# Optimization experiments

Measured on AMD Instinct MI355X. Metric: run time of the kernel, lower is better.

The kernel has to match this reference:

```python
import jax, jax.numpy as jnp
import numpy as np

N_NODES = 50000
N_EDGES = 800000
IN_CH, HID_CH, OUT_CH, HEADS = 64, 32, 64, 8
NEG_SLOPE = 0.2


def setup_inputs() -> dict:
    key = jax.random.key(0)
    ks = jax.random.split(key, 12)
    x = jax.random.normal(ks[0], (N_NODES, IN_CH), dtype=jnp.float32)
    src = jax.random.randint(ks[1], (N_EDGES,), 0, N_NODES)
    dst = jax.random.randint(ks[2], (N_EDGES,), 0, N_NODES)
    edge_index = jnp.stack([src, dst]).astype(jnp.int64)
    g1 = 1.0 / np.sqrt(IN_CH)
    g2 = 1.0 / np.sqrt(HID_CH * HEADS)
    W1 = jax.random.normal(ks[3], (IN_CH, HEADS * HID_CH), dtype=jnp.float32) * g1
    a1_src = jax.random.normal(ks[4], (HEADS, HID_CH), dtype=jnp.float32) * g1
    a1_dst = jax.random.normal(ks[5], (HEADS, HID_CH), dtype=jnp.float32) * g1
    b1 = jnp.zeros((HEADS * HID_CH,), dtype=jnp.float32)
    W2 = jax.random.normal(ks[6], (HEADS * HID_CH, OUT_CH), dtype=jnp.float32) * g2
    a2_src = jax.random.normal(ks[7], (1, OUT_CH), dtype=jnp.float32) * g2
    a2_dst = jax.random.normal(ks[8], (1, OUT_CH), dtype=jnp.float32) * g2
    b2 = jnp.zeros((OUT_CH,), dtype=jnp.float32)
    return {"x": x, "edge_index": edge_index, "W1": W1, "a1_src": a1_src,
            "a1_dst": a1_dst, "b1": b1, "W2": W2, "a2_src": a2_src,
            "a2_dst": a2_dst, "b2": b2}


def _gat_conv(x, src, dst, W, a_s, a_d, b, heads, out_ch, concat):
    """PyG GATConv: per-head linear, edge attention, segment softmax, scatter-add."""
    n = x.shape[0]
    h = (x @ W).reshape(n, heads, out_ch)                    # [N,H,C]
    al_s = jnp.einsum('nhc,hc->nh', h, a_s)                  # [N,H]
    al_d = jnp.einsum('nhc,hc->nh', h, a_d)
    e = jax.nn.leaky_relu(al_s[src] + al_d[dst], NEG_SLOPE)  # [E,H]
    m = jax.ops.segment_max(e, dst, num_segments=n)          # [N,H]
    m = jnp.where(jnp.isfinite(m), m, 0.0)
    ex = jnp.exp(e - m[dst])
    denom = jax.ops.segment_sum(ex, dst, num_segments=n)
    alpha = ex / (denom[dst] + 1e-16)                        # [E,H]
    msg = h[src] * alpha[:, :, None]                         # [E,H,C]
    out = jax.ops.segment_sum(msg, dst, num_segments=n)      # [N,H,C]
    out = out.reshape(n, heads * out_ch) if concat else out.mean(axis=1)
    return out + b


def reference(x, edge_index, W1, a1_src, a1_dst, b1, W2, a2_src, a2_dst, b2):
    n = x.shape[0]
    loops = jnp.arange(n, dtype=edge_index.dtype)
    src = jnp.concatenate([edge_index[0], loops])  # self-loops (PyG default)
    dst = jnp.concatenate([edge_index[1], loops])
    h = _gat_conv(x, src, dst, W1, a1_src, a1_dst, b1, HEADS, HID_CH, True)
    h = jax.nn.elu(h)
    return _gat_conv(h, src, dst, W2, a2_src, a2_dst, b2, 1, OUT_CH, False)
```

## Files before the change

kernel.cpp:

```cpp
#include <hip/hip_runtime.h>
#include <hip/hip_fp16.h>

#define NEG_SLOPE 0.2f
#define CAP 64
#define EPB 4096
#define CAP_B 2560

__global__ __launch_bounds__(256, 4) void k_phase1(
    const int* __restrict__ ei, int E,
    const float* __restrict__ x, const float* __restrict__ W1,
    const float* __restrict__ a1s, const float* __restrict__ a1d,
    __half* __restrict__ h1h, float* __restrict__ al1s, float* __restrict__ al1d,
    int* __restrict__ cursor, unsigned* __restrict__ pairs,
    int n, int nbuck, int nP1B)
{
  __shared__ int sh[2048];
  int t = threadIdx.x;
  if (blockIdx.x < nP1B) {
    int* hist = sh;
    int* hbase = sh + 512;
    for (int i = t; i < nbuck; i += 256) hist[i] = 0;
    __syncthreads();
    int ebase = blockIdx.x * EPB;
    int pk[16], bk[16], rk[16];
#pragma unroll
    for (int k = 0; k < 16; k++) {
      int eid = ebase + k * 256 + t;
      bk[k] = -1; pk[k] = 0; rk[k] = 0;
      if (eid < E) {
        int s = ei[eid], d = ei[E + eid];
        s = (s < 0) ? 0 : (s >= n ? n - 1 : s);
        d = (d < 0) ? 0 : (d >= n ? n - 1 : d);
        bk[k] = d >> 7;
        pk[k] = ((d & 127) << 17) | s;
        rk[k] = atomicAdd(&hist[d >> 7], 1);
      }
    }
    __syncthreads();
    for (int b = t; b < nbuck; b += 256) {
      int c = hist[b];
      hbase[b] = c ? atomicAdd(&cursor[b], c) : 0;
    }
    __syncthreads();
#pragma unroll
    for (int k = 0; k < 16; k++) {
      if (bk[k] >= 0) {
        int idx = hbase[bk[k]] + rk[k];
        if (idx < CAP_B)
          pairs[(size_t)bk[k] * CAP_B + idx] = (unsigned)pk[k];
      }
    }
    return;
  }
  float (*xs)[64] = reinterpret_cast<float(*)[64]>(sh);
  int cg = t & 63;
  int mg = t >> 6;
  int base = (blockIdx.x - nP1B) * 32;
  for (int i = t; i < 32 * 16; i += 256) {
    int m = i >> 4, k4 = i & 15;
    int node = base + m;
    float4 v = make_float4(0.f, 0.f, 0.f, 0.f);
    if (node < n) v = reinterpret_cast<const float4*>(x + (size_t)node * 64)[k4];
    reinterpret_cast<float4*>(&xs[m][0])[k4] = v;
  }
  float4 as4 = reinterpret_cast<const float4*>(a1s)[cg];
  float4 ad4 = reinterpret_cast<const float4*>(a1d)[cg];
  __syncthreads();
  float4 acc[8];
#pragma unroll
  for (int m = 0; m < 8; m++) acc[m] = make_float4(0.f, 0.f, 0.f, 0.f);
#pragma unroll 1
  for (int k4 = 0; k4 < 16; k4++) {
    float4 w0 = reinterpret_cast<const float4*>(W1 + (size_t)(4 * k4 + 0) * 256)[cg];
    float4 w1 = reinterpret_cast<const float4*>(W1 + (size_t)(4 * k4 + 1) * 256)[cg];
    float4 w2 = reinterpret_cast<const float4*>(W1 + (size_t)(4 * k4 + 2) * 256)[cg];
    float4 w3 = reinterpret_cast<const float4*>(W1 + (size_t)(4 * k4 + 3) * 256)[cg];
#pragma unroll
    for (int m = 0; m < 8; m++) {
      float4 xv = reinterpret_cast<float4*>(&xs[mg * 8 + m][0])[k4];
      acc[m].x = fmaf(xv.x, w0.x, acc[m].x); acc[m].y = fmaf(xv.x, w0.y, acc[m].y);
      acc[m].z = fmaf(xv.x, w0.z, acc[m].z); acc[m].w = fmaf(xv.x, w0.w, acc[m].w);
      acc[m].x = fmaf(xv.y, w1.x, acc[m].x); acc[m].y = fmaf(xv.y, w1.y, acc[m].y);
      acc[m].z = fmaf(xv.y, w1.z, acc[m].z); acc[m].w = fmaf(xv.y, w1.w, acc[m].w);
      acc[m].x = fmaf(xv.z, w2.x, acc[m].x); acc[m].y = fmaf(xv.z, w2.y, acc[m].y);
      acc[m].z = fmaf(xv.z, w2.z, acc[m].z); acc[m].w = fmaf(xv.z, w2.w, acc[m].w);
      acc[m].x = fmaf(xv.w, w3.x, acc[m].x); acc[m].y = fmaf(xv.w, w3.y, acc[m].y);
      acc[m].z = fmaf(xv.w, w3.z, acc[m].z); acc[m].w = fmaf(xv.w, w3.w, acc[m].w);
    }
  }
#pragma unroll
  for (int m = 0; m < 8; m++) {
    int node = base + mg * 8 + m;
    if (node < n) {
      __half2 p01 = __floats2half2_rn(acc[m].x, acc[m].y);
      __half2 p23 = __floats2half2_rn(acc[m].z, acc[m].w);
      uint2 pko;
      pko.x = *reinterpret_cast<unsigned int*>(&p01);
      pko.y = *reinterpret_cast<unsigned int*>(&p23);
      reinterpret_cast<uint2*>(h1h + (size_t)node * 256)[cg] = pko;
      float s_ = acc[m].x * as4.x + acc[m].y * as4.y + acc[m].z * as4.z + acc[m].w * as4.w;
      float d_ = acc[m].x * ad4.x + acc[m].y * ad4.y + acc[m].z * ad4.z + acc[m].w * ad4.w;
      s_ += __shfl_xor(s_, 1); d_ += __shfl_xor(d_, 1);
      s_ += __shfl_xor(s_, 2); d_ += __shfl_xor(d_, 2);
      s_ += __shfl_xor(s_, 4); d_ += __shfl_xor(d_, 4);
      if ((cg & 7) == 0) {
        al1s[node * 8 + (cg >> 3)] = s_;
        al1d[node * 8 + (cg >> 3)] = d_;
      }
    }
  }
}

__global__ __launch_bounds__(256) void k_pass2(
    const unsigned* __restrict__ pairs, const int* __restrict__ cursor,
    int* __restrict__ deg, int* __restrict__ esrc, int n)
{
  __shared__ int cnt[128];
  int b = blockIdx.x, t = threadIdx.x;
  if (t < 128) cnt[t] = 0;
  __syncthreads();
  int total = min(cursor[b], CAP_B);
  size_t base = (size_t)b * CAP_B;
  for (int i = t; i < total; i += 256) {
    unsigned p = pairs[base + i];
    int s = p & 0x1FFFF;
    int local = p >> 17;
    int slot = atomicAdd(&cnt[local], 1);
    if (slot < CAP) esrc[((b << 7) + local) * CAP + slot] = s;
  }
  __syncthreads();
  if (t < 128) {
    int node = (b << 7) + t;
    if (node < n) deg[node] = min(cnt[t], CAP);
  }
}

__global__ __launch_bounds__(256, 4) void k_linear2(
    const __half* __restrict__ hacth, const float* __restrict__ W2,
    const float* __restrict__ a2s, const float* __restrict__ a2d,
    __half* __restrict__ h2h, float* __restrict__ al2s, float* __restrict__ al2d,
    int n)
{
  __shared__ float xs[32][260];
  int t = threadIdx.x;
  int cg = t & 15;
  int mg = t >> 4;
  int base = blockIdx.x * 32;
  for (int i = t; i < 32 * 32; i += 256) {
    int m = i >> 5, c8 = i & 31;
    int node = base + m;
    uint4 pk = make_uint4(0, 0, 0, 0);
    if (node < n) pk = reinterpret_cast<const uint4*>(hacth + (size_t)node * 256)[c8];
    __half2* hp = reinterpret_cast<__half2*>(&pk);
    float2 f0 = __half22float2(hp[0]);
    float2 f1 = __half22float2(hp[1]);
    float2 f2 = __half22float2(hp[2]);
    float2 f3 = __half22float2(hp[3]);
    float4* dst = reinterpret_cast<float4*>(&xs[m][c8 * 8]);
    dst[0] = make_float4(f0.x, f0.y, f1.x, f1.y);
    dst[1] = make_float4(f2.x, f2.y, f3.x, f3.y);
  }
  float4 as4 = reinterpret_cast<const float4*>(a2s)[cg];
  float4 ad4 = reinterpret_cast<const float4*>(a2d)[cg];
  __syncthreads();
  float4 a0 = make_float4(0.f, 0.f, 0.f, 0.f);
  float4 a1 = make_float4(0.f, 0.f, 0.f, 0.f);
#pragma unroll 2
  for (int k4 = 0; k4 < 64; k4++) {
    float4 w0 = reinterpret_cast<const float4*>(W2 + (size_t)(4 * k4 + 0) * 64)[cg];
    float4 w1 = reinterpret_cast<const float4*>(W2 + (size_t)(4 * k4 + 1) * 64)[cg];
    float4 w2 = reinterpret_cast<const float4*>(W2 + (size_t)(4 * k4 + 2) * 64)[cg];
    float4 w3 = reinterpret_cast<const float4*>(W2 + (size_t)(4 * k4 + 3) * 64)[cg];
    float4 x0 = *reinterpret_cast<float4*>(&xs[2 * mg + 0][k4 * 4]);
    float4 x1 = *reinterpret_cast<float4*>(&xs[2 * mg + 1][k4 * 4]);
    a0.x = fmaf(x0.x, w0.x, a0.x); a0.y = fmaf(x0.x, w0.y, a0.y);
    a0.z = fmaf(x0.x, w0.z, a0.z); a0.w = fmaf(x0.x, w0.w, a0.w);
    a0.x = fmaf(x0.y, w1.x, a0.x); a0.y = fmaf(x0.y, w1.y, a0.y);
    a0.z = fmaf(x0.y, w1.z, a0.z); a0.w = fmaf(x0.y, w1.w, a0.w);
    a0.x = fmaf(x0.z, w2.x, a0.x); a0.y = fmaf(x0.z, w2.y, a0.y);
    a0.z = fmaf(x0.z, w2.z, a0.z); a0.w = fmaf(x0.z, w2.w, a0.w);
    a0.x = fmaf(x0.w, w3.x, a0.x); a0.y = fmaf(x0.w, w3.y, a0.y);
    a0.z = fmaf(x0.w, w3.z, a0.z); a0.w = fmaf(x0.w, w3.w, a0.w);
    a1.x = fmaf(x1.x, w0.x, a1.x); a1.y = fmaf(x1.x, w0.y, a1.y);
    a1.z = fmaf(x1.x, w0.z, a1.z); a1.w = fmaf(x1.x, w0.w, a1.w);
    a1.x = fmaf(x1.y, w1.x, a1.x); a1.y = fmaf(x1.y, w1.y, a1.y);
    a1.z = fmaf(x1.y, w1.z, a1.z); a1.w = fmaf(x1.y, w1.w, a1.w);
    a1.x = fmaf(x1.z, w2.x, a1.x); a1.y = fmaf(x1.z, w2.y, a1.y);
    a1.z = fmaf(x1.z, w2.z, a1.z); a1.w = fmaf(x1.z, w2.w, a1.w);
    a1.x = fmaf(x1.w, w3.x, a1.x); a1.y = fmaf(x1.w, w3.y, a1.y);
    a1.z = fmaf(x1.w, w3.z, a1.z); a1.w = fmaf(x1.w, w3.w, a1.w);
  }
#pragma unroll
  for (int nd = 0; nd < 2; nd++) {
    float4 a = nd ? a1 : a0;
    int node = base + 2 * mg + nd;
    if (node < n) {
      __half2 q0 = __floats2half2_rn(a.x, a.y);
      __half2 q1 = __floats2half2_rn(a.z, a.w);
      uint2 pk;
      pk.x = *reinterpret_cast<unsigned int*>(&q0);
      pk.y = *reinterpret_cast<unsigned int*>(&q1);
      reinterpret_cast<uint2*>(h2h + (size_t)node * 64)[cg] = pk;
      float s_ = a.x * as4.x + a.y * as4.y + a.z * as4.z + a.w * as4.w;
      float d_ = a.x * ad4.x + a.y * ad4.y + a.z * ad4.z + a.w * ad4.w;
      s_ += __shfl_xor(s_, 1); d_ += __shfl_xor(d_, 1);
      s_ += __shfl_xor(s_, 2); d_ += __shfl_xor(d_, 2);
      s_ += __shfl_xor(s_, 4); d_ += __shfl_xor(d_, 4);
      s_ += __shfl_xor(s_, 8); d_ += __shfl_xor(d_, 8);
      if (cg == 0) { al2s[node] = s_; al2d[node] = d_; }
    }
  }
}

__global__ __launch_bounds__(256) void k_gather1(
    const __half* __restrict__ h1h, const float* __restrict__ al1s, const float* __restrict__ al1d,
    const int* __restrict__ degv, const int* __restrict__ esrc,
    const float* __restrict__ b1, __half* __restrict__ hacth, int n)
{
  int node = blockIdx.x * 16 + (threadIdx.x >> 4);
  if (node >= n) return;
  int q = threadIdx.x & 15;
  int head = q >> 1;
  int beg = node * CAP;
  int deg = min(degv[node], CAP);
  float ald = al1d[node * 8 + head];
  const uint4* rowN = reinterpret_cast<const uint4*>(h1h + (size_t)node * 256);
  uint4 n0 = rowN[2 * q], n1 = rowN[2 * q + 1];
  float eS = al1s[node * 8 + head] + ald;
  eS = eS > 0.f ? eS : NEG_SLOPE * eS;
  float exS = __expf(eS);
  float acc[16];
#pragma unroll
  for (int k = 0; k < 16; k++) acc[k] = 0.f;
  float den = 0.f;
  if (deg > 0) {
    int sA = esrc[beg];
    float alA = al1s[sA * 8 + head];
    const uint4* rowA = reinterpret_cast<const uint4*>(h1h + (size_t)sA * 256);
    uint4 pa0 = rowA[2 * q], pa1 = rowA[2 * q + 1];
    for (int i = 0; i < deg; i++) {
      float alB = 0.f;
      uint4 pb0 = make_uint4(0, 0, 0, 0), pb1 = make_uint4(0, 0, 0, 0);
      if (i + 1 < deg) {
        int sB = esrc[beg + i + 1];
        alB = al1s[sB * 8 + head];
        const uint4* rowB = reinterpret_cast<const uint4*>(h1h + (size_t)sB * 256);
        pb0 = rowB[2 * q]; pb1 = rowB[2 * q + 1];
      }
      float e = alA + ald;
      e = e > 0.f ? e : NEG_SLOPE * e;
      float ex = __expf(e);
      den += ex;
      __half2* hp0 = reinterpret_cast<__half2*>(&pa0);
      __half2* hp1 = reinterpret_cast<__half2*>(&pa1);
#pragma unroll
      for (int j = 0; j < 4; j++) {
        float2 f0 = __half22float2(hp0[j]);
        float2 f1 = __half22float2(hp1[j]);
        acc[2 * j + 0] = fmaf(ex, f0.x, acc[2 * j + 0]);
        acc[2 * j + 1] = fmaf(ex, f0.y, acc[2 * j + 1]);
        acc[8 + 2 * j + 0] = fmaf(ex, f1.x, acc[8 + 2 * j + 0]);
        acc[8 + 2 * j + 1] = fmaf(ex, f1.y, acc[8 + 2 * j + 1]);
      }
      alA = alB; pa0 = pb0; pa1 = pb1;
    }
  }
  den += exS;
  {
    __half2* hp0 = reinterpret_cast<__half2*>(&n0);
    __half2* hp1 = reinterpret_cast<__half2*>(&n1);
#pragma unroll
    for (int j = 0; j < 4; j++) {
      float2 f0 = __half22float2(hp0[j]);
      float2 f1 = __half22float2(hp1[j]);
      acc[2 * j + 0] = fmaf(exS, f0.x, acc[2 * j + 0]);
      acc[2 * j + 1] = fmaf(exS, f0.y, acc[2 * j + 1]);
      acc[8 + 2 * j + 0] = fmaf(exS, f1.x, acc[8 + 2 * j + 0]);
      acc[8 + 2 * j + 1] = fmaf(exS, f1.y, acc[8 + 2 * j + 1]);
    }
  }
  float inv = 1.f / (den + 1e-16f);
  float o[16];
#pragma unroll
  for (int j = 0; j < 4; j++) {
    float4 b4 = reinterpret_cast<const float4*>(b1)[4 * q + j];
    o[4 * j + 0] = acc[4 * j + 0] * inv + b4.x;
    o[4 * j + 1] = acc[4 * j + 1] * inv + b4.y;
    o[4 * j + 2] = acc[4 * j + 2] * inv + b4.z;
    o[4 * j + 3] = acc[4 * j + 3] * inv + b4.w;
  }
#pragma unroll
  for (int k = 0; k < 16; k++) o[k] = o[k] > 0.f ? o[k] : (__expf(o[k]) - 1.f);
  uint4 w0, w1;
  __half2 t0, t1;
  t0 = __floats2half2_rn(o[0], o[1]);  w0.x = *reinterpret_cast<unsigned int*>(&t0);
  t1 = __floats2half2_rn(o[2], o[3]);  w0.y = *reinterpret_cast<unsigned int*>(&t1);
  t0 = __floats2half2_rn(o[4], o[5]);  w0.z = *reinterpret_cast<unsigned int*>(&t0);
  t1 = __floats2half2_rn(o[6], o[7]);  w0.w = *reinterpret_cast<unsigned int*>(&t1);
  t0 = __floats2half2_rn(o[8], o[9]);  w1.x = *reinterpret_cast<unsigned int*>(&t0);
  t1 = __floats2half2_rn(o[10], o[11]); w1.y = *reinterpret_cast<unsigned int*>(&t1);
  t0 = __floats2half2_rn(o[12], o[13]); w1.z = *reinterpret_cast<unsigned int*>(&t0);
  t1 = __floats2half2_rn(o[14], o[15]); w1.w = *reinterpret_cast<unsigned int*>(&t1);
  uint4* orow = reinterpret_cast<uint4*>(hacth + (size_t)node * 256);
  orow[2 * q] = w0; orow[2 * q + 1] = w1;
}

__global__ __launch_bounds__(256) void k_gather2(
    const __half* __restrict__ h2h, const float* __restrict__ al2s, const float* __restrict__ al2d,
    const int* __restrict__ degv, const int* __restrict__ esrc,
    const float* __restrict__ b2, float* __restrict__ out, int n)
{
  int node = blockIdx.x * 32 + (threadIdx.x >> 3);
  if (node >= n) return;
  int q = threadIdx.x & 7;
  int beg = node * CAP;
  int deg = min(degv[node], CAP);
  float ald = al2d[node];
  uint4 pN = reinterpret_cast<const uint4*>(h2h + (size_t)node * 64)[q];
  float eS = al2s[node] + ald;
  eS = eS > 0.f ? eS : NEG_SLOPE * eS;
  float exS = __expf(eS);
  float acc[8];
#pragma unroll
  for (int k = 0; k < 8; k++) acc[k] = 0.f;
  float den = 0.f;
  if (deg > 0) {
    int sA = esrc[beg];
    float alA = al2s[sA];
    uint4 pA = reinterpret_cast<const uint4*>(h2h + (size_t)sA * 64)[q];
    for (int i = 0; i < deg; i++) {
      float alB = 0.f;
      uint4 pB = make_uint4(0, 0, 0, 0);
      if (i + 1 < deg) {
        int sB = esrc[beg + i + 1];
        alB = al2s[sB];
        pB = reinterpret_cast<const uint4*>(h2h + (size_t)sB * 64)[q];
      }
      float e = alA + ald;
      e = e > 0.f ? e : NEG_SLOPE * e;
      float ex = __expf(e);
      den += ex;
      __half2* hp = reinterpret_cast<__half2*>(&pA);
#pragma unroll
      for (int j = 0; j < 4; j++) {
        float2 f = __half22float2(hp[j]);
        acc[2 * j + 0] = fmaf(ex, f.x, acc[2 * j + 0]);
        acc[2 * j + 1] = fmaf(ex, f.y, acc[2 * j + 1]);
      }
      alA = alB; pA = pB;
    }
  }
  den += exS;
  {
    __half2* hp = reinterpret_cast<__half2*>(&pN);
#pragma unroll
    for (int j = 0; j < 4; j++) {
      float2 f = __half22float2(hp[j]);
      acc[2 * j + 0] = fmaf(exS, f.x, acc[2 * j + 0]);
      acc[2 * j + 1] = fmaf(exS, f.y, acc[2 * j + 1]);
    }
  }
  float inv = 1.f / (den + 1e-16f);
  float4 b40 = reinterpret_cast<const float4*>(b2)[2 * q];
  float4 b41 = reinterpret_cast<const float4*>(b2)[2 * q + 1];
  float4 o0, o1;
  o0.x = acc[0] * inv + b40.x; o0.y = acc[1] * inv + b40.y;
  o0.z = acc[2] * inv + b40.z; o0.w = acc[3] * inv + b40.w;
  o1.x = acc[4] * inv + b41.x; o1.y = acc[5] * inv + b41.y;
  o1.z = acc[6] * inv + b41.z; o1.w = acc[7] * inv + b41.w;
  float4* orow = reinterpret_cast<float4*>(out + (size_t)node * 64);
  orow[2 * q] = o0; orow[2 * q + 1] = o1;
}

extern "C" void kernel_launch(void* const* d_in, const int* in_sizes, int n_in,
                              void* d_out, int out_size, void* d_ws, size_t ws_size,
                              hipStream_t stream)
{
  const float* x        = (const float*)d_in[0];
  const int*   ei       = (const int*)d_in[1];
  const float* W1       = (const float*)d_in[2];
  const float* a1s      = (const float*)d_in[3];
  const float* a1d      = (const float*)d_in[4];
  const float* b1       = (const float*)d_in[5];
  const float* W2       = (const float*)d_in[6];
  const float* a2s      = (const float*)d_in[7];
  const float* a2d      = (const float*)d_in[8];
  const float* b2       = (const float*)d_in[9];
  float* out            = (float*)d_out;

  int N  = in_sizes[0] / 64;
  int E  = in_sizes[1] / 2;
  int NBUCK = (N + 127) >> 7;

  char* p = (char*)d_ws;
  auto alloc = [&](size_t bytes) -> char* {
    char* r = p;
    p += (bytes + 255) & ~(size_t)255;
    return r;
  };
  __half* h1h    = (__half*)alloc((size_t)N * 256 * 2);
  __half* hacth  = (__half*)alloc((size_t)N * 256 * 2);
  float* al1s    = (float*)alloc((size_t)N * 8 * 4);
  float* al1d    = (float*)alloc((size_t)N * 8 * 4);
  float* al2s    = (float*)alloc((size_t)N * 4);
  float* al2d    = (float*)alloc((size_t)N * 4);
  int*   deg     = (int*)alloc((size_t)N * 4);
  int*   esrc    = (int*)alloc((size_t)N * CAP * 4);
  unsigned* pairs = (unsigned*)alloc((size_t)NBUCK * CAP_B * 4);
  int*   cursor  = (int*)alloc((size_t)NBUCK * 4);
  __half* h2h    = h1h;

  hipMemsetAsync(cursor, 0, (size_t)NBUCK * 4, stream);

  int nP1B = (E + EPB - 1) / EPB;
  int nLB = (N + 31) / 32;
  k_phase1<<<nP1B + nLB, 256, 0, stream>>>(ei, E, x, W1, a1s, a1d,
                                           h1h, al1s, al1d, cursor, pairs, N, NBUCK, nP1B);
  k_pass2<<<NBUCK, 256, 0, stream>>>(pairs, cursor, deg, esrc, N);
  k_gather1<<<(N + 15) / 16, 256, 0, stream>>>(h1h, al1s, al1d, deg, esrc, b1, hacth, N);
  k_linear2<<<(N + 31) / 32, 256, 0, stream>>>(hacth, W2, a2s, a2d, h2h, al2s, al2d, N);
  k_gather2<<<(N + 31) / 32, 256, 0, stream>>>(h2h, al2s, al2d, deg, esrc, b2, out, N);
}
```

Baseline: 206.2 us.

## Use head-major feature slabs and compact CSR adjacency for the layer-1 gather

The layer-1 projected features and attention logits are stored head-major, so each head forms a contiguous 32-channel slab. The layer-1 gather now runs one block per head per 64 nodes, which keeps each head's slab smaller and more cache-resident during random source lookups. The fixed CAP=64 padded adjacency is replaced by a compact CSR built with a per-bucket prefix sum and a global atomic offset, which also drops the degree cap. The cost is an extra pass over the pairs in pass2, and each source's index and degree are now read eight times, once per head.

```diff
diff --git a/kernel.cpp b/kernel.cpp
--- a/kernel.cpp
+++ b/kernel.cpp
@@ -2,7 +2,6 @@
 #include <hip/hip_fp16.h>
 
 #define NEG_SLOPE 0.2f
-#define CAP 64
 #define EPB 4096
 #define CAP_B 2560
 
@@ -92,20 +91,21 @@
   for (int m = 0; m < 8; m++) {
     int node = base + mg * 8 + m;
     if (node < n) {
+      int head = cg >> 3;
       __half2 p01 = __floats2half2_rn(acc[m].x, acc[m].y);
       __half2 p23 = __floats2half2_rn(acc[m].z, acc[m].w);
       uint2 pko;
       pko.x = *reinterpret_cast<unsigned int*>(&p01);
       pko.y = *reinterpret_cast<unsigned int*>(&p23);
-      reinterpret_cast<uint2*>(h1h + (size_t)node * 256)[cg] = pko;
+      reinterpret_cast<uint2*>(h1h + (size_t)head * n * 32 + (size_t)node * 32)[cg & 7] = pko;
       float s_ = acc[m].x * as4.x + acc[m].y * as4.y + acc[m].z * as4.z + acc[m].w * as4.w;
       float d_ = acc[m].x * ad4.x + acc[m].y * ad4.y + acc[m].z * ad4.z + acc[m].w * ad4.w;
       s_ += __shfl_xor(s_, 1); d_ += __shfl_xor(d_, 1);
       s_ += __shfl_xor(s_, 2); d_ += __shfl_xor(d_, 2);
       s_ += __shfl_xor(s_, 4); d_ += __shfl_xor(d_, 4);
       if ((cg & 7) == 0) {
-        al1s[node * 8 + (cg >> 3)] = s_;
-        al1d[node * 8 + (cg >> 3)] = d_;
+        al1s[(size_t)head * n + node] = s_;
+        al1d[(size_t)head * n + node] = d_;
       }
     }
   }
@@ -113,25 +113,35 @@
 
 __global__ __launch_bounds__(256) void k_pass2(
     const unsigned* __restrict__ pairs, const int* __restrict__ cursor,
-    int* __restrict__ deg, int* __restrict__ esrc, int n)
-{
-  __shared__ int cnt[128];
+    int* __restrict__ gcur, int* __restrict__ deg, int* __restrict__ rowoff,
+    int* __restrict__ csr, int n)
+{
+  __shared__ int cnt[128], off[128], rk[128];
+  __shared__ int bbase;
   int b = blockIdx.x, t = threadIdx.x;
-  if (t < 128) cnt[t] = 0;
+  if (t < 128) { cnt[t] = 0; rk[t] = 0; }
   __syncthreads();
   int total = min(cursor[b], CAP_B);
   size_t base = (size_t)b * CAP_B;
+  for (int i = t; i < total; i += 256)
+    atomicAdd(&cnt[pairs[base + i] >> 17], 1);
+  __syncthreads();
+  if (t == 0) {
+    int run = 0;
+    for (int i = 0; i < 128; i++) { off[i] = run; run += cnt[i]; }
+    bbase = atomicAdd(gcur, run);
+  }
+  __syncthreads();
+  int bb = bbase;
+  if (t < 128) {
+    int node = (b << 7) + t;
+    if (node < n) { deg[node] = cnt[t]; rowoff[node] = bb + off[t]; }
+  }
   for (int i = t; i < total; i += 256) {
     unsigned p = pairs[base + i];
-    int s = p & 0x1FFFF;
     int local = p >> 17;
-    int slot = atomicAdd(&cnt[local], 1);
-    if (slot < CAP) esrc[((b << 7) + local) * CAP + slot] = s;
-  }
-  __syncthreads();
-  if (t < 128) {
-    int node = (b << 7) + t;
-    if (node < n) deg[node] = min(cnt[t], CAP);
+    int slot = atomicAdd(&rk[local], 1);
+    csr[bb + off[local] + slot] = (int)(p & 0x1FFFF);
   }
 }
 
@@ -214,107 +224,92 @@
 
 __global__ __launch_bounds__(256) void k_gather1(
     const __half* __restrict__ h1h, const float* __restrict__ al1s, const float* __restrict__ al1d,
-    const int* __restrict__ degv, const int* __restrict__ esrc,
+    const int* __restrict__ degv, const int* __restrict__ rowoff, const int* __restrict__ csr,
     const float* __restrict__ b1, __half* __restrict__ hacth, int n)
 {
-  int node = blockIdx.x * 16 + (threadIdx.x >> 4);
+  int head = blockIdx.x & 7;
+  int node = ((blockIdx.x >> 3) << 6) + (threadIdx.x >> 2);
   if (node >= n) return;
-  int q = threadIdx.x & 15;
-  int head = q >> 1;
-  int beg = node * CAP;
-  int deg = min(degv[node], CAP);
-  float ald = al1d[node * 8 + head];
-  const uint4* rowN = reinterpret_cast<const uint4*>(h1h + (size_t)node * 256);
-  uint4 n0 = rowN[2 * q], n1 = rowN[2 * q + 1];
-  float eS = al1s[node * 8 + head] + ald;
+  int q = threadIdx.x & 2 ? (threadIdx.x & 3) : (threadIdx.x & 3);
+  q = threadIdx.x & 3;
+  const __half* slab = h1h + (size_t)head * n * 32;
+  const float* als = al1s + (size_t)head * n;
+  float ald = al1d[(size_t)head * n + node];
+  int beg = rowoff[node];
+  int deg = degv[node];
+  uint4 nr = reinterpret_cast<const uint4*>(slab + (size_t)node * 32)[q];
+  float eS = als[node] + ald;
   eS = eS > 0.f ? eS : NEG_SLOPE * eS;
   float exS = __expf(eS);
-  float acc[16];
-#pragma unroll
-  for (int k = 0; k < 16; k++) acc[k] = 0.f;
+  float acc[8];
+#pragma unroll
+  for (int k = 0; k < 8; k++) acc[k] = 0.f;
   float den = 0.f;
   if (deg > 0) {
-    int sA = esrc[beg];
-    float alA = al1s[sA * 8 + head];
-    const uint4* rowA = reinterpret_cast<const uint4*>(h1h + (size_t)sA * 256);
-    uint4 pa0 = rowA[2 * q], pa1 = rowA[2 * q + 1];
+    int sA = csr[beg];
+    float alA = als[sA];
+    uint4 pa = reinterpret_cast<const uint4*>(slab + (size_t)sA * 32)[q];
     for (int i = 0; i < deg; i++) {
       float alB = 0.f;
-      uint4 pb0 = make_uint4(0, 0, 0, 0), pb1 = make_uint4(0, 0, 0, 0);
+      uint4 pb = make_uint4(0, 0, 0, 0);
       if (i + 1 < deg) {
-        int sB = esrc[beg + i + 1];
-        alB = al1s[sB * 8 + head];
-        const uint4* rowB = reinterpret_cast<const uint4*>(h1h + (size_t)sB * 256);
-        pb0 = rowB[2 * q]; pb1 = rowB[2 * q + 1];
+        int sB = csr[beg + i + 1];
+        alB = als[sB];
+        pb = reinterpret_cast<const uint4*>(slab + (size_t)sB * 32)[q];
       }
       float e = alA + ald;
       e = e > 0.f ? e : NEG_SLOPE * e;
       float ex = __expf(e);
       den += ex;
-      __half2* hp0 = reinterpret_cast<__half2*>(&pa0);
-      __half2* hp1 = reinterpret_cast<__half2*>(&pa1);
+      __half2* hp = reinterpret_cast<__half2*>(&pa);
 #pragma unroll
       for (int j = 0; j < 4; j++) {
-        float2 f0 = __half22float2(hp0[j]);
-        float2 f1 = __half22float2(hp1[j]);
-        acc[2 * j + 0] = fmaf(ex, f0.x, acc[2 * j + 0]);
-        acc[2 * j + 1] = fmaf(ex, f0.y, acc[2 * j + 1]);
-        acc[8 + 2 * j + 0] = fmaf(ex, f1.x, acc[8 + 2 * j + 0]);
-        acc[8 + 2 * j + 1] = fmaf(ex, f1.y, acc[8 + 2 * j + 1]);
-      }
-      alA = alB; pa0 = pb0; pa1 = pb1;
+        float2 f = __half22float2(hp[j]);
+        acc[2 * j + 0] = fmaf(ex, f.x, acc[2 * j + 0]);
+        acc[2 * j + 1] = fmaf(ex, f.y, acc[2 * j + 1]);
+      }
+      alA = alB; pa = pb;
     }
   }
   den += exS;
   {
-    __half2* hp0 = reinterpret_cast<__half2*>(&n0);
-    __half2* hp1 = reinterpret_cast<__half2*>(&n1);
+    __half2* hp = reinterpret_cast<__half2*>(&nr);
 #pragma unroll
     for (int j = 0; j < 4; j++) {
-      float2 f0 = __half22float2(hp0[j]);
-      float2 f1 = __half22float2(hp1[j]);
-      acc[2 * j + 0] = fmaf(exS, f0.x, acc[2 * j + 0]);
-      acc[2 * j + 1] = fmaf(exS, f0.y, acc[2 * j + 1]);
-      acc[8 + 2 * j + 0] = fmaf(exS, f1.x, acc[8 + 2 * j + 0]);
-      acc[8 + 2 * j + 1] = fmaf(exS, f1.y, acc[8 + 2 * j + 1]);
+      float2 f = __half22float2(hp[j]);
+      acc[2 * j + 0] = fmaf(exS, f.x, acc[2 * j + 0]);
+      acc[2 * j + 1] = fmaf(exS, f.y, acc[2 * j + 1]);
     }
   }
   float inv = 1.f / (den + 1e-16f);
-  float o[16];
-#pragma unroll
-  for (int j = 0; j < 4; j++) {
-    float4 b4 = reinterpret_cast<const float4*>(b1)[4 * q + j];
-    o[4 * j + 0] = acc[4 * j + 0] * inv + b4.x;
-    o[4 * j + 1] = acc[4 * j + 1] * inv + b4.y;
-    o[4 * j + 2] = acc[4 * j + 2] * inv + b4.z;
-    o[4 * j + 3] = acc[4 * j + 3] * inv + b4.w;
-  }
-#pragma unroll
-  for (int k = 0; k < 16; k++) o[k] = o[k] > 0.f ? o[k] : (__expf(o[k]) - 1.f);
-  uint4 w0, w1;
+  float4 b40 = reinterpret_cast<const float4*>(b1 + head * 32)[2 * q];
+  float4 b41 = reinterpret_cast<const float4*>(b1 + head * 32)[2 * q + 1];
+  float o[8];
+  o[0] = acc[0] * inv + b40.x; o[1] = acc[1] * inv + b40.y;
+  o[2] = acc[2] * inv + b40.z; o[3] = acc[3] * inv + b40.w;
+  o[4] = acc[4] * inv + b41.x; o[5] = acc[5] * inv + b41.y;
+  o[6] = acc[6] * inv + b41.z; o[7] = acc[7] * inv + b41.w;
+#pragma unroll
+  for (int k = 0; k < 8; k++) o[k] = o[k] > 0.f ? o[k] : (__expf(o[k]) - 1.f);
+  uint4 w0;
   __half2 t0, t1;
   t0 = __floats2half2_rn(o[0], o[1]);  w0.x = *reinterpret_cast<unsigned int*>(&t0);
   t1 = __floats2half2_rn(o[2], o[3]);  w0.y = *reinterpret_cast<unsigned int*>(&t1);
   t0 = __floats2half2_rn(o[4], o[5]);  w0.z = *reinterpret_cast<unsigned int*>(&t0);
   t1 = __floats2half2_rn(o[6], o[7]);  w0.w = *reinterpret_cast<unsigned int*>(&t1);
-  t0 = __floats2half2_rn(o[8], o[9]);  w1.x = *reinterpret_cast<unsigned int*>(&t0);
-  t1 = __floats2half2_rn(o[10], o[11]); w1.y = *reinterpret_cast<unsigned int*>(&t1);
-  t0 = __floats2half2_rn(o[12], o[13]); w1.z = *reinterpret_cast<unsigned int*>(&t0);
-  t1 = __floats2half2_rn(o[14], o[15]); w1.w = *reinterpret_cast<unsigned int*>(&t1);
-  uint4* orow = reinterpret_cast<uint4*>(hacth + (size_t)node * 256);
-  orow[2 * q] = w0; orow[2 * q + 1] = w1;
+  *reinterpret_cast<uint4*>(hacth + (size_t)node * 256 + head * 32 + q * 8) = w0;
 }
 
 __global__ __launch_bounds__(256) void k_gather2(
     const __half* __restrict__ h2h, const float* __restrict__ al2s, const float* __restrict__ al2d,
-    const int* __restrict__ degv, const int* __restrict__ esrc,
+    const int* __restrict__ degv, const int* __restrict__ rowoff, const int* __restrict__ csr,
     const float* __restrict__ b2, float* __restrict__ out, int n)
 {
   int node = blockIdx.x * 32 + (threadIdx.x >> 3);
   if (node >= n) return;
   int q = threadIdx.x & 7;
-  int beg = node * CAP;
-  int deg = min(degv[node], CAP);
+  int beg = rowoff[node];
+  int deg = degv[node];
   float ald = al2d[node];
   uint4 pN = reinterpret_cast<const uint4*>(h2h + (size_t)node * 64)[q];
   float eS = al2s[node] + ald;
@@ -325,14 +320,14 @@
   for (int k = 0; k < 8; k++) acc[k] = 0.f;
   float den = 0.f;
   if (deg > 0) {
-    int sA = esrc[beg];
+    int sA = csr[beg];
     float alA = al2s[sA];
     uint4 pA = reinterpret_cast<const uint4*>(h2h + (size_t)sA * 64)[q];
     for (int i = 0; i < deg; i++) {
       float alB = 0.f;
       uint4 pB = make_uint4(0, 0, 0, 0);
       if (i + 1 < deg) {
-        int sB = esrc[beg + i + 1];
+        int sB = csr[beg + i + 1];
         alB = al2s[sB];
         pB = reinterpret_cast<const uint4*>(h2h + (size_t)sB * 64)[q];
       }
@@ -405,19 +400,22 @@
   float* al2s    = (float*)alloc((size_t)N * 4);
   float* al2d    = (float*)alloc((size_t)N * 4);
   int*   deg     = (int*)alloc((size_t)N * 4);
-  int*   esrc    = (int*)alloc((size_t)N * CAP * 4);
+  int*   rowoff  = (int*)alloc((size_t)N * 4);
+  int*   csr     = (int*)alloc((size_t)NBUCK * CAP_B * 4);
   unsigned* pairs = (unsigned*)alloc((size_t)NBUCK * CAP_B * 4);
-  int*   cursor  = (int*)alloc((size_t)NBUCK * 4);
+  int*   cursor  = (int*)alloc((size_t)(NBUCK + 1) * 4);
+  int*   gcur    = cursor + NBUCK;
   __half* h2h    = h1h;
 
-  hipMemsetAsync(cursor, 0, (size_t)NBUCK * 4, stream);
+  hipMemsetAsync(cursor, 0, (size_t)(NBUCK + 1) * 4, stream);
 
   int nP1B = (E + EPB - 1) / EPB;
   int nLB = (N + 31) / 32;
   k_phase1<<<nP1B + nLB, 256, 0, stream>>>(ei, E, x, W1, a1s, a1d,
                                            h1h, al1s, al1d, cursor, pairs, N, NBUCK, nP1B);
-  k_pass2<<<NBUCK, 256, 0, stream>>>(pairs, cursor, deg, esrc, N);
-  k_gather1<<<(N + 15) / 16, 256, 0, stream>>>(h1h, al1s, al1d, deg, esrc, b1, hacth, N);
+  k_pass2<<<NBUCK, 256, 0, stream>>>(pairs, cursor, gcur, deg, rowoff, csr, N);
+  int nG1 = 8 * ((N + 63) / 64);
+  k_gather1<<<nG1, 256, 0, stream>>>(h1h, al1s, al1d, deg, rowoff, csr, b1, hacth, N);
   k_linear2<<<(N + 31) / 32, 256, 0, stream>>>(hacth, W2, a2s, a2d, h2h, al2s, al2d, N);
-  k_gather2<<<(N + 31) / 32, 256, 0, stream>>>(h2h, al2s, al2d, deg, esrc, b2, out, N);
-}
+  k_gather2<<<(N + 31) / 32, 256, 0, stream>>>(h2h, al2s, al2d, deg, rowoff, csr, b2, out, N);
+}
```

Result: slower. 232.7 us (+12.9%).
